# Optimization experiments

Measured on AMD Instinct MI355X. Metric: run time of the kernel, lower is better.

The kernel has to match this reference:

```python
import jax, jax.numpy as jnp
import numpy as np
import math

B, L, D = 2, 2048, 1024
H, HD = 16, 64          # num heads, head dim
R = 256                 # kv lora rank = D // 4
E, K, F = 8, 2, 1024    # routed experts, top_k, intermediate size


def rmsnorm(x, w, eps=1e-6):
    ms = jnp.mean(x * x, axis=-1, keepdims=True)
    return w * (x * jax.lax.rsqrt(ms + eps))


def setup_inputs() -> dict:
    key = jax.random.key(0)
    ks = jax.random.split(key, 16)
    s = 0.02
    return {
        "x": jax.random.normal(ks[0], (B, L, D), jnp.float32),
        "ln1_w": jnp.ones((D,), jnp.float32),
        "q_w": jax.random.normal(ks[1], (D, H * HD), jnp.float32) * s,
        "kvd_w": jax.random.normal(ks[2], (D, R), jnp.float32) * s,
        "kvn_w": jnp.ones((R,), jnp.float32),
        "kvu_w": jax.random.normal(ks[3], (R, 2 * H * HD), jnp.float32) * s,
        "o_w": jax.random.normal(ks[4], (H * HD, D), jnp.float32) * s,
        "ln2_w": jnp.ones((D,), jnp.float32),
        "gate_w": jax.random.normal(ks[5], (D, E), jnp.float32) * s,
        "sh_w1": jax.random.normal(ks[6], (D, F), jnp.float32) * s,
        "sh_w2": jax.random.normal(ks[7], (F, D), jnp.float32) * s,
        "sh_w3": jax.random.normal(ks[8], (D, F), jnp.float32) * s,
        "re_w1": jax.random.normal(ks[9], (E, D, F), jnp.float32) * s,
        "re_w2": jax.random.normal(ks[10], (E, F, D), jnp.float32) * s,
        "re_w3": jax.random.normal(ks[11], (E, D, F), jnp.float32) * s,
    }


def reference(x, ln1_w, q_w, kvd_w, kvn_w, kvu_w, o_w, ln2_w, gate_w,
              sh_w1, sh_w2, sh_w3, re_w1, re_w2, re_w3):
    # ---- MLHA attention with pre-RMSNorm and latent-compressed KV ----
    xn = rmsnorm(x, ln1_w)
    q = (xn @ q_w).reshape(B, L, H, HD)
    latent = rmsnorm(xn @ kvd_w, kvn_w)                 # [B,L,R]
    kv = latent @ kvu_w                                 # [B,L,2*H*HD]
    k, v = jnp.split(kv, 2, axis=-1)
    k = k.reshape(B, L, H, HD)
    v = v.reshape(B, L, H, HD)
    scores = jnp.einsum('bxhd,byhd->bhxy', q, k) / math.sqrt(HD)
    causal = jnp.tril(jnp.ones((L, L), bool))
    scores = jnp.where(causal, scores, -jnp.inf)
    attn = jax.nn.softmax(scores, axis=-1)
    attn_out = jnp.einsum('bhxy,byhd->bxhd', attn, v).reshape(B, L, H * HD)
    h = x + attn_out @ o_w

    # ---- MoE (inference: no jitter, expert_bias = 0, no bias update) ----
    hn = rmsnorm(h, ln2_w)
    flat = hn.reshape(-1, D)                            # [T,D], T=B*L
    # shared expert (SwiGLU)
    shared = (jax.nn.silu(flat @ sh_w1) * (flat @ sh_w3)) @ sh_w2
    # router
    logits = flat @ gate_w                              # [T,E]
    probs = jax.nn.softmax(logits, axis=-1)
    topw, topi = jax.lax.top_k(probs, K)                # [T,K]
    topw = topw / jnp.sum(topw, axis=-1, keepdims=True)
    # per-token per-expert combine weight [T,E]
    combine = jnp.sum(topw[..., None] * jax.nn.one_hot(topi, E, dtype=flat.dtype), axis=1)
    # all routed experts densely, then masked combine (same math as masked loop)
    h1 = jnp.einsum('td,edf->etf', flat, re_w1)
    h3 = jnp.einsum('td,edf->etf', flat, re_w3)
    eo = jnp.einsum('etf,efd->etd', jax.nn.silu(h1) * h3, re_w2)
    routed = jnp.einsum('te,etd->td', combine, eo)
    moe_out = (shared + routed).reshape(B, L, D)
    return h + moe_out, probs
```

## Files before the change

kernel.cpp:

```cpp
#include <hip/hip_runtime.h>
#include <hip/hip_bf16.h>
#include <cstdint>
#include <cstddef>

typedef unsigned short u16;
typedef unsigned int u32;
typedef __attribute__((ext_vector_type(8))) short bf16x8;
typedef __attribute__((ext_vector_type(4))) float f32x4;

static constexpr int Bb = 2, Ll = 2048, Dd = 1024, Hh = 16, Rr = 256, Ee = 8, Ff = 1024;
static constexpr int Tt = Bb * Ll;

__device__ __forceinline__ u16 f2bf(float f){
  union { float f; u32 u; } v; v.f = f;
  u32 u = v.u;
  u32 r = u + 0x7FFFu + ((u >> 16) & 1u);
  return (u16)(r >> 16);
}
__device__ __forceinline__ float bf2f(u16 b){
  union { u32 u; float f; } v; v.u = ((u32)b) << 16; return v.f;
}

#define GLDS(gp, lp) __builtin_amdgcn_global_load_lds( \
    (const __attribute__((address_space(1))) unsigned int*)(gp), \
    (__attribute__((address_space(3))) unsigned int*)(lp), 16, 0, 0)

__global__ void transpose_conv(const float* __restrict__ src, u16* __restrict__ dst,
                               int K, int N, int SN, int dstOff){
  __shared__ float tile[32][33];
  const float* s = src + (size_t)blockIdx.z * K * N;
  int bx = blockIdx.x * 32;
  int by = blockIdx.y * 32;
  int tx = threadIdx.x, ty = threadIdx.y;
  #pragma unroll
  for (int i = ty; i < 32; i += 8) tile[i][tx] = s[(size_t)(by + i) * N + bx + tx];
  __syncthreads();
  size_t rowbase = (size_t)blockIdx.z * SN + dstOff + bx;
  #pragma unroll
  for (int i = ty; i < 32; i += 8) dst[(rowbase + i) * K + by + tx] = f2bf(tile[tx][i]);
}

template<int DIM>
__global__ void rmsnorm_kernel(const float* __restrict__ x, const float* __restrict__ w,
                               u16* __restrict__ out){
  int t = blockIdx.x;
  const float* xr = x + (size_t)t * DIM;
  u16* orow = out + (size_t)t * DIM;
  int tid = threadIdx.x;
  constexpr int NT = 256;
  constexpr int PER = DIM / NT > 0 ? DIM / NT : 1;
  float vals[PER];
  float ss = 0.f;
  #pragma unroll
  for (int i = 0; i < PER; i++){
    int d = tid + i * NT;
    float v = (d < DIM) ? xr[d] : 0.f;
    vals[i] = v; ss += v * v;
  }
  __shared__ float red[4];
  for (int m = 32; m; m >>= 1) ss += __shfl_xor(ss, m, 64);
  if ((tid & 63) == 0) red[tid >> 6] = ss;
  __syncthreads();
  float tot = red[0] + red[1] + red[2] + red[3];
  float rn = rsqrtf(tot / DIM + 1e-6f);
  #pragma unroll
  for (int i = 0; i < PER; i++){
    int d = tid + i * NT;
    if (d < DIM) orow[d] = f2bf(vals[i] * rn * w[d]);
  }
}

__global__ void router_kernel(const float* __restrict__ h, const float* __restrict__ ln2w,
                              const float* __restrict__ gate,
                              float* __restrict__ probs_out,
                              int* __restrict__ topi, float* __restrict__ topw){
  int t = blockIdx.x; int tid = threadIdx.x;
  const float* hr = h + (size_t)t * Dd;
  float v[4]; float ss = 0.f;
  #pragma unroll
  for (int i = 0; i < 4; i++){ float x = hr[tid + i * 256]; v[i] = x; ss += x * x; }
  __shared__ float red[4];
  for (int m = 32; m; m >>= 1) ss += __shfl_xor(ss, m, 64);
  if ((tid & 63) == 0) red[tid >> 6] = ss;
  __syncthreads();
  float rn = rsqrtf((red[0] + red[1] + red[2] + red[3]) / Dd + 1e-6f);
  float p[8];
  #pragma unroll
  for (int e = 0; e < 8; e++) p[e] = 0.f;
  #pragma unroll
  for (int i = 0; i < 4; i++){
    int d = tid + i * 256;
    float hv = v[i] * rn * ln2w[d];
    const float* g = gate + (size_t)d * 8;
    #pragma unroll
    for (int e = 0; e < 8; e++) p[e] += hv * g[e];
  }
  #pragma unroll
  for (int e = 0; e < 8; e++){
    float x = p[e];
    for (int m = 32; m; m >>= 1) x += __shfl_xor(x, m, 64);
    p[e] = x;
  }
  __shared__ float pe[4][8];
  if ((tid & 63) == 0){ for (int e = 0; e < 8; e++) pe[tid >> 6][e] = p[e]; }
  __syncthreads();
  if (tid == 0){
    float lg[8];
    for (int e = 0; e < 8; e++) lg[e] = pe[0][e] + pe[1][e] + pe[2][e] + pe[3][e];
    float mx = lg[0];
    for (int e = 1; e < 8; e++) mx = fmaxf(mx, lg[e]);
    float pr[8]; float s = 0.f;
    for (int e = 0; e < 8; e++){ pr[e] = __expf(lg[e] - mx); s += pr[e]; }
    float inv = 1.f / s;
    for (int e = 0; e < 8; e++) probs_out[(size_t)t * 8 + e] = pr[e] * inv;
    int i0 = 0;
    for (int e = 1; e < 8; e++) if (pr[e] > pr[i0]) i0 = e;
    int i1 = -1;
    for (int e = 0; e < 8; e++){ if (e == i0) continue; if (i1 < 0 || pr[e] > pr[i1]) i1 = e; }
    float w0 = pr[i0], w1 = pr[i1]; float wn = 1.f / (w0 + w1);
    topi[t * 2] = i0; topi[t * 2 + 1] = i1;
    topw[t * 2] = w0 * wn; topw[t * 2 + 1] = w1 * wn;
  }
}

__global__ void hist_kernel(const int* __restrict__ topi, int* __restrict__ counts){
  __shared__ int h[8];
  int tid = threadIdx.x;
  if (tid < 8) h[tid] = 0;
  __syncthreads();
  int base = blockIdx.x * 512;
  for (int i = tid; i < 512; i += 256) atomicAdd(&h[topi[base + i]], 1);
  __syncthreads();
  if (tid < 8) atomicAdd(&counts[tid], h[tid]);
}

__global__ void scan_kernel(const int* __restrict__ counts, int* __restrict__ offs){
  if (threadIdx.x == 0 && blockIdx.x == 0){
    int c = 0;
    for (int e = 0; e < 8; e++){ offs[e] = c; c += counts[e]; }
  }
}

__global__ void bucket_kernel(const int* __restrict__ topi, const float* __restrict__ topw,
                              const int* __restrict__ offs, int* __restrict__ cur,
                              int* __restrict__ entries, float* __restrict__ ew){
  __shared__ int lh[8], lbase[8], lcur[8];
  int tid = threadIdx.x;
  if (tid < 8) lh[tid] = 0;
  __syncthreads();
  int t = blockIdx.x * 256 + tid;
  int e0 = topi[t * 2], e1 = topi[t * 2 + 1];
  atomicAdd(&lh[e0], 1); atomicAdd(&lh[e1], 1);
  __syncthreads();
  if (tid < 8){ lbase[tid] = atomicAdd(&cur[tid], lh[tid]); lcur[tid] = 0; }
  __syncthreads();
  int p0 = atomicAdd(&lcur[e0], 1);
  int pos0 = offs[e0] + lbase[e0] + p0;
  entries[pos0] = t; ew[pos0] = topw[t * 2];
  int p1 = atomicAdd(&lcur[e1], 1);
  int pos1 = offs[e1] + lbase[e1] + p1;
  entries[pos1] = t; ew[pos1] = topw[t * 2 + 1];
}

__global__ void swiglu_kernel(u16* __restrict__ buf, int rows){
  int idx = blockIdx.x * 256 + threadIdx.x;
  int t = idx >> 7, f = (idx & 127) * 8;
  if (t >= rows) return;
  u16* p = buf + (size_t)t * 2048 + f;
  bf16x8 a = *(const bf16x8*)p;
  bf16x8 b = *(const bf16x8*)(p + 1024);
  bf16x8 o;
  #pragma unroll
  for (int j = 0; j < 8; j++){
    float av = bf2f(((const u16*)&a)[j]);
    float bv = bf2f(((const u16*)&b)[j]);
    float s = av / (1.f + __expf(-av));
    ((u16*)&o)[j] = f2bf(s * bv);
  }
  *(bf16x8*)p = o;
}

template<int TM, int ROWMODE, int MODE>
__launch_bounds__(256)
__global__ void gemm_bt(const u16* __restrict__ A, const u16* __restrict__ Bt,
                        void* __restrict__ C, const float* __restrict__ res,
                        int M, int N, int K, int lda, int ldc,
                        const int* __restrict__ entries, const float* __restrict__ ew,
                        const int* __restrict__ counts, const int* __restrict__ offs,
                        float* __restrict__ outAt){
  constexpr int MTC = TM / 32;
  __shared__ __align__(16) u16 As[TM * 32];
  __shared__ __align__(16) u16 Bs[128 * 32];
  __shared__ int els[TM];
  __shared__ float ewl[TM];

  int e = (ROWMODE ? blockIdx.z : 0);
  const u16* Bte = Bt + (size_t)e * N * K;
  int cnt, off;
  if (ROWMODE == 0){ cnt = M; off = 0; }
  else { cnt = counts[e]; off = offs[e]; }
  int rt = blockIdx.y * TM;
  if (rt >= cnt) return;
  int cb = blockIdx.x * 128;
  int tid = threadIdx.x;

  if (ROWMODE >= 1){
    if (tid < TM){
      int r = rt + tid;
      els[tid] = (r < cnt) ? entries[off + r] : 0;
      ewl[tid] = (MODE == 4 && r < cnt) ? ew[off + r] : 0.f;
    }
    __syncthreads();
  }

  int sr = tid >> 2;
  int skc = (tid & 3) * 8;
  int rr0 = rt + sr, rr1 = rt + sr + 64;
  size_t ar0 = 0, ar1 = 0;
  if (ROWMODE == 0){ ar0 = (size_t)rr0; ar1 = (size_t)rr1; }
  else if (ROWMODE == 1){ ar0 = (size_t)els[sr];
                          ar1 = (TM == 128) ? (size_t)els[sr + 64] : 0; }
  else {
    int c0 = rr0 < cnt ? rr0 : (cnt - 1);
    int c1 = rr1 < cnt ? rr1 : (cnt - 1);
    ar0 = (size_t)off + c0; ar1 = (size_t)off + c1;
  }
  const u16* pa0 = A + ar0 * lda + skc;
  const u16* pa1 = A + ar1 * lda + skc;
  const u16* pb0 = Bte + (size_t)(cb + sr) * K + skc;
  const u16* pb1 = Bte + (size_t)(cb + sr + 64) * K + skc;
  u16* lA0 = &As[tid * 8];
  u16* lA1 = &As[(TM == 128 ? 2048 : 0) + tid * 8];
  u16* lB0 = &Bs[tid * 8];
  u16* lB1 = &Bs[2048 + tid * 8];

  int w = tid >> 6, lane = tid & 63;
  int wm = w >> 1, wn = w & 1;
  int quad = lane >> 4, l16 = lane & 15;

  f32x4 acc[MTC][4];
  const f32x4 zf = {0.f, 0.f, 0.f, 0.f};
  #pragma unroll
  for (int i = 0; i < MTC; i++)
    #pragma unroll
    for (int j = 0; j < 4; j++) acc[i][j] = zf;

  for (int k0 = 0; k0 < K; k0 += 32){
    __syncthreads();
    GLDS(pa0 + k0, lA0);
    if (TM == 128) GLDS(pa1 + k0, lA1);
    GLDS(pb0 + k0, lB0);
    GLDS(pb1 + k0, lB1);
    __syncthreads();
    bf16x8 af[MTC], bfr[4];
    #pragma unroll
    for (int mt = 0; mt < MTC; mt++)
      af[mt] = *(const bf16x8*)&As[(wm * (TM / 2) + mt * 16 + l16) * 32 + quad * 8];
    #pragma unroll
    for (int nt = 0; nt < 4; nt++)
      bfr[nt] = *(const bf16x8*)&Bs[(wn * 64 + nt * 16 + l16) * 32 + quad * 8];
    #pragma unroll
    for (int mt = 0; mt < MTC; mt++)
      #pragma unroll
      for (int nt = 0; nt < 4; nt++)
        acc[mt][nt] = __builtin_amdgcn_mfma_f32_16x16x32_bf16(af[mt], bfr[nt], acc[mt][nt], 0, 0, 0);
  }

  #pragma unroll
  for (int mt = 0; mt < MTC; mt++){
    #pragma unroll
    for (int nt = 0; nt < 4; nt++){
      #pragma unroll
      for (int r = 0; r < 4; r++){
        int row = wm * (TM / 2) + mt * 16 + quad * 4 + r;
        int col = cb + wn * 64 + nt * 16 + l16;
        int rr = rt + row;
        if (rr >= cnt) continue;
        float v = acc[mt][nt][r];
        if (MODE == 0){
          size_t ci = (size_t)((ROWMODE == 1) ? (off + rr) : rr) * ldc + col;
          ((u16*)C)[ci] = f2bf(v);
        } else if (MODE == 1){
          size_t ci = (size_t)rr * ldc + col;
          ((float*)C)[ci] = v + res[ci];
        } else if (MODE == 5){
          if (col < 1024) ((u16*)C)[(size_t)rr * 1024 + col] = f2bf(v);
          else            outAt[(size_t)rr * 256 + (col - 1024)] = v;
        } else {
          int tok = els[row];
          atomicAdd(&outAt[(size_t)tok * ldc + col], ewl[row] * v);
        }
      }
    }
  }
}

__global__ void vt_kernel(const u16* __restrict__ kv, u16* __restrict__ vt){
  __shared__ __align__(16) u16 t[64 * 72];
  int kt = blockIdx.x * 64, h = blockIdx.y, b = blockIdx.z;
  size_t bL = (size_t)b * Ll;
  int tid = threadIdx.x;
  int r = tid >> 2, c0 = (tid & 3) * 16;
  const u16* src = kv + (bL + kt + r) * 2048 + 1024 + h * 64 + c0;
  *(uint4*)&t[r * 72 + c0]     = *(const uint4*)(src);
  *(uint4*)&t[r * 72 + c0 + 8] = *(const uint4*)(src + 8);
  __syncthreads();
  int d = tid >> 2; int k0 = (tid & 3) * 16;
  u16 tmp[16];
  #pragma unroll
  for (int j = 0; j < 16; j++) tmp[j] = t[(k0 + j) * 72 + d];
  u16* dst = vt + ((size_t)(b * Hh + h) * 64 + d) * (size_t)Ll + kt + k0;
  *(uint4*)dst       = *(const uint4*)&tmp[0];
  *(uint4*)(dst + 8) = *(const uint4*)&tmp[8];
}

__launch_bounds__(256)
__global__ void attn_kernel(const u16* __restrict__ q, const u16* __restrict__ kv,
                            const u16* __restrict__ vt, u16* __restrict__ out){
  constexpr int LD = 72;
  __shared__ __align__(16) u16 Ks[64 * LD];
  __shared__ __align__(16) u16 Vs[64 * LD];
  __shared__ __align__(16) u16 Ps[64 * LD];
  int q0 = blockIdx.x * 64, h = blockIdx.y, b = blockIdx.z;
  size_t bL = (size_t)b * Ll;
  int tid = threadIdx.x, w = tid >> 6, lane = tid & 63, quad = lane >> 4, l16 = lane & 15;
  int qrow = q0 + w * 16 + l16;

  bf16x8 qf[2];
  #pragma unroll
  for (int ks = 0; ks < 2; ks++)
    qf[ks] = *(const bf16x8*)(q + (bL + qrow) * 1024 + h * 64 + ks * 32 + quad * 8);

  f32x4 oacc[4];
  const f32x4 zf = {0.f, 0.f, 0.f, 0.f};
  #pragma unroll
  for (int dt = 0; dt < 4; dt++) oacc[dt] = zf;
  float mprev = -1e30f, lsum = 0.f;

  int sr = tid >> 2, sc = (tid & 3) * 16;
  const u16* kbase = kv + (bL + sr) * 2048 + h * 64 + sc;
  const u16* vbase = vt + ((size_t)(b * Hh + h) * 64 + sr) * (size_t)Ll + sc;

  for (int kt = 0; kt <= q0; kt += 64){
    __syncthreads();
    {
      const u16* kp = kbase + (size_t)kt * 2048;
      *(uint4*)&Ks[sr * LD + sc]     = *(const uint4*)(kp);
      *(uint4*)&Ks[sr * LD + sc + 8] = *(const uint4*)(kp + 8);
      const u16* vp = vbase + kt;
      *(uint4*)&Vs[sr * LD + sc]     = *(const uint4*)(vp);
      *(uint4*)&Vs[sr * LD + sc + 8] = *(const uint4*)(vp + 8);
    }
    __syncthreads();

    f32x4 sacc[4];
    #pragma unroll
    for (int mt = 0; mt < 4; mt++) sacc[mt] = zf;
    #pragma unroll
    for (int ks = 0; ks < 2; ks++){
      #pragma unroll
      for (int mt = 0; mt < 4; mt++){
        bf16x8 kf = *(const bf16x8*)&Ks[(mt * 16 + l16) * LD + ks * 32 + quad * 8];
        sacc[mt] = __builtin_amdgcn_mfma_f32_16x16x32_bf16(kf, qf[ks], sacc[mt], 0, 0, 0);
      }
    }
    bool diag = (kt == q0);
    int lq = w * 16 + l16;
    float sv[16]; float mx = -1e30f;
    #pragma unroll
    for (int mt = 0; mt < 4; mt++){
      #pragma unroll
      for (int r = 0; r < 4; r++){
        float s = sacc[mt][r] * 0.125f;
        if (diag && (mt * 16 + quad * 4 + r > lq)) s = -1e30f;
        sv[mt * 4 + r] = s;
        mx = fmaxf(mx, s);
      }
    }
    mx = fmaxf(mx, __shfl_xor(mx, 16, 64));
    mx = fmaxf(mx, __shfl_xor(mx, 32, 64));
    float mnew = fmaxf(mprev, mx);
    float alpha = __expf(mprev - mnew);
    mprev = mnew;
    float rs = 0.f;
    #pragma unroll
    for (int mt = 0; mt < 4; mt++){
      ushort4 pk;
      float p0 = __expf(sv[mt * 4 + 0] - mnew);
      float p1 = __expf(sv[mt * 4 + 1] - mnew);
      float p2 = __expf(sv[mt * 4 + 2] - mnew);
      float p3 = __expf(sv[mt * 4 + 3] - mnew);
      rs += p0 + p1 + p2 + p3;
      pk.x = f2bf(p0); pk.y = f2bf(p1); pk.z = f2bf(p2); pk.w = f2bf(p3);
      *(ushort4*)&Ps[(w * 16 + l16) * LD + mt * 16 + quad * 4] = pk;
    }
    rs += __shfl_xor(rs, 16, 64);
    rs += __shfl_xor(rs, 32, 64);
    lsum = lsum * alpha + rs;
    #pragma unroll
    for (int dt = 0; dt < 4; dt++) oacc[dt] *= alpha;

    #pragma unroll
    for (int ks = 0; ks < 2; ks++){
      bf16x8 pf = *(const bf16x8*)&Ps[(w * 16 + l16) * LD + ks * 32 + quad * 8];
      #pragma unroll
      for (int dt = 0; dt < 4; dt++){
        bf16x8 vf = *(const bf16x8*)&Vs[(dt * 16 + l16) * LD + ks * 32 + quad * 8];
        oacc[dt] = __builtin_amdgcn_mfma_f32_16x16x32_bf16(vf, pf, oacc[dt], 0, 0, 0);
      }
    }
  }

  float inv = 1.f / lsum;
  #pragma unroll
  for (int dt = 0; dt < 4; dt++){
    ushort4 ov;
    ov.x = f2bf(oacc[dt][0] * inv);
    ov.y = f2bf(oacc[dt][1] * inv);
    ov.z = f2bf(oacc[dt][2] * inv);
    ov.w = f2bf(oacc[dt][3] * inv);
    *(ushort4*)(out + (bL + qrow) * 1024 + h * 64 + dt * 16 + quad * 4) = ov;
  }
}

extern "C" void kernel_launch(void* const* d_in, const int* in_sizes, int n_in,
                              void* d_out, int out_size, void* d_ws, size_t ws_size,
                              hipStream_t stream){
  const float* x     = (const float*)d_in[0];
  const float* ln1_w = (const float*)d_in[1];
  const float* q_w   = (const float*)d_in[2];
  const float* kvd_w = (const float*)d_in[3];
  const float* kvn_w = (const float*)d_in[4];
  const float* kvu_w = (const float*)d_in[5];
  const float* o_w   = (const float*)d_in[6];
  const float* ln2_w = (const float*)d_in[7];
  const float* gate_w= (const float*)d_in[8];
  const float* sh_w1 = (const float*)d_in[9];
  const float* sh_w2 = (const float*)d_in[10];
  const float* sh_w3 = (const float*)d_in[11];
  const float* re_w1 = (const float*)d_in[12];
  const float* re_w2 = (const float*)d_in[13];
  const float* re_w3 = (const float*)d_in[14];
  float* out = (float*)d_out;

  char* wp = (char*)d_ws;
  auto alloc = [&](size_t bytes)->char*{
    char* p = wp; wp += (bytes + 255) & ~(size_t)255; return p;
  };
  u16* qkvdT = (u16*)alloc((size_t)1280 * 1024 * 2);
  u16* kvuT  = (u16*)alloc((size_t)2048 * 256 * 2);
  u16* oT    = (u16*)alloc((size_t)1024 * 1024 * 2);
  u16* sh13T = (u16*)alloc((size_t)2048 * 1024 * 2);
  u16* sh2T  = (u16*)alloc((size_t)1024 * 1024 * 2);
  u16* re13T = (u16*)alloc((size_t)8 * 2048 * 1024 * 2);
  u16* re2T  = (u16*)alloc((size_t)8 * 1024 * 1024 * 2);
  u16* xn    = (u16*)alloc((size_t)Tt * 1024 * 2);
  u16* qbuf  = (u16*)alloc((size_t)Tt * 1024 * 2);
  float* latpre = (float*)alloc((size_t)Tt * 256 * 4);
  u16* lat   = (u16*)alloc((size_t)Tt * 256 * 2);
  u16* kvbuf = (u16*)alloc((size_t)Tt * 2048 * 2);
  u16* attnb = (u16*)alloc((size_t)Tt * 1024 * 2);
  float* hbuf = (float*)alloc((size_t)Tt * 1024 * 4);
  u16* vtb   = (u16*)alloc((size_t)Bb * Hh * 64 * Ll * 2);
  u16* h13r  = (u16*)alloc((size_t)Tt * 2 * 2048 * 2);
  int* counts = (int*)alloc(32);
  int* cur    = (int*)alloc(32);
  int* offs   = (int*)alloc(32);
  int* topi   = (int*)alloc((size_t)Tt * 2 * 4);
  float* topw = (float*)alloc((size_t)Tt * 2 * 4);
  int* entries= (int*)alloc((size_t)Tt * 2 * 4);
  float* ewt  = (float*)alloc((size_t)Tt * 2 * 4);
  (void)ws_size; (void)n_in; (void)in_sizes; (void)out_size;

  hipMemsetAsync(counts, 0, 32, stream);
  hipMemsetAsync(cur, 0, 32, stream);

  dim3 tb(32, 8);
  transpose_conv<<<dim3(32, 32, 1), tb, 0, stream>>>(q_w,   qkvdT, 1024, 1024, 1280, 0);
  transpose_conv<<<dim3(8,  32, 1), tb, 0, stream>>>(kvd_w, qkvdT, 1024, 256,  1280, 1024);
  transpose_conv<<<dim3(64, 8,  1), tb, 0, stream>>>(kvu_w, kvuT,  256,  2048, 2048, 0);
  transpose_conv<<<dim3(32, 32, 1), tb, 0, stream>>>(o_w,   oT,    1024, 1024, 1024, 0);
  transpose_conv<<<dim3(32, 32, 1), tb, 0, stream>>>(sh_w1, sh13T, 1024, 1024, 2048, 0);
  transpose_conv<<<dim3(32, 32, 1), tb, 0, stream>>>(sh_w3, sh13T, 1024, 1024, 2048, 1024);
  transpose_conv<<<dim3(32, 32, 1), tb, 0, stream>>>(sh_w2, sh2T,  1024, 1024, 1024, 0);
  transpose_conv<<<dim3(32, 32, 8), tb, 0, stream>>>(re_w1, re13T, 1024, 1024, 2048, 0);
  transpose_conv<<<dim3(32, 32, 8), tb, 0, stream>>>(re_w3, re13T, 1024, 1024, 2048, 1024);
  transpose_conv<<<dim3(32, 32, 8), tb, 0, stream>>>(re_w2, re2T,  1024, 1024, 1024, 0);

  rmsnorm_kernel<1024><<<Tt, 256, 0, stream>>>(x, ln1_w, xn);

  gemm_bt<64,0,5><<<dim3(10, 64), 256, 0, stream>>>(xn, qkvdT, qbuf, nullptr,
      Tt, 1280, 1024, 1024, 1024, nullptr, nullptr, nullptr, nullptr, latpre);
  rmsnorm_kernel<256><<<Tt, 256, 0, stream>>>(latpre, kvn_w, lat);
  gemm_bt<128,0,0><<<dim3(16, 32), 256, 0, stream>>>(lat, kvuT, kvbuf, nullptr,
      Tt, 2048, 256, 256, 2048, nullptr, nullptr, nullptr, nullptr, nullptr);
  vt_kernel<<<dim3(32, 16, 2), 256, 0, stream>>>(kvbuf, vtb);
  attn_kernel<<<dim3(32, 16, 2), 256, 0, stream>>>(qbuf, kvbuf, vtb, attnb);
  gemm_bt<64,0,1><<<dim3(8, 64), 256, 0, stream>>>(attnb, oT, hbuf, x,
      Tt, 1024, 1024, 1024, 1024, nullptr, nullptr, nullptr, nullptr, nullptr);
  rmsnorm_kernel<1024><<<Tt, 256, 0, stream>>>(hbuf, ln2_w, xn);
  router_kernel<<<Tt, 256, 0, stream>>>(hbuf, ln2_w, gate_w, out + (size_t)Tt * Dd,
                                        topi, topw);
  hist_kernel<<<16, 256, 0, stream>>>(topi, counts);
  scan_kernel<<<1, 64, 0, stream>>>(counts, offs);
  bucket_kernel<<<16, 256, 0, stream>>>(topi, topw, offs, cur, entries, ewt);

  gemm_bt<128,0,0><<<dim3(16, 32), 256, 0, stream>>>(xn, sh13T, kvbuf, nullptr,
      Tt, 2048, 1024, 1024, 2048, nullptr, nullptr, nullptr, nullptr, nullptr);
  swiglu_kernel<<<Tt / 2, 256, 0, stream>>>(kvbuf, Tt);
  gemm_bt<64,0,1><<<dim3(8, 64), 256, 0, stream>>>(kvbuf, sh2T, out, hbuf,
      Tt, 1024, 1024, 2048, 1024, nullptr, nullptr, nullptr, nullptr, nullptr);

  gemm_bt<128,1,0><<<dim3(16, 32, 8), 256, 0, stream>>>(xn, re13T, h13r, nullptr,
      Tt, 2048, 1024, 1024, 2048, entries, nullptr, counts, offs, nullptr);
  swiglu_kernel<<<Tt, 256, 0, stream>>>(h13r, 2 * Tt);
  gemm_bt<128,2,4><<<dim3(8, 32, 8), 256, 0, stream>>>(h13r, re2T, nullptr, nullptr,
      Tt, 1024, 1024, 2048, 1024, entries, ewt, counts, offs, out);
}
```

Before: 608.6 us.

## Fuse SwiGLU into GEMM epilogues, merge transposes, balance causal attention blocks

```diff
diff --git a/kernel.cpp b/kernel.cpp
--- a/kernel.cpp
+++ b/kernel.cpp
@@ -25,19 +25,61 @@
     (const __attribute__((address_space(1))) unsigned int*)(gp), \
     (__attribute__((address_space(3))) unsigned int*)(lp), 16, 0, 0)
 
+__global__ void transpose5(const float* __restrict__ q_w, const float* __restrict__ o_w,
+                           const float* __restrict__ w1, const float* __restrict__ w3,
+                           const float* __restrict__ w2,
+                           u16* __restrict__ qkvdT, u16* __restrict__ oT,
+                           u16* __restrict__ sh13T, u16* __restrict__ sh2T){
+  const float* s; u16* d; int off, str;
+  switch (blockIdx.z){
+    case 0: s = q_w; d = qkvdT; off = 0; str = 1; break;
+    case 1: s = o_w; d = oT;    off = 0; str = 1; break;
+    case 2: s = w1;  d = sh13T; off = 0; str = 2; break;
+    case 3: s = w3;  d = sh13T; off = 1; str = 2; break;
+    default: s = w2; d = sh2T;  off = 0; str = 1; break;
+  }
+  __shared__ float tile[32][33];
+  int bx = blockIdx.x * 32, by = blockIdx.y * 32;
+  int tx = threadIdx.x, ty = threadIdx.y;
+  #pragma unroll
+  for (int i = ty; i < 32; i += 8) tile[i][tx] = s[(size_t)(by + i) * 1024 + bx + tx];
+  __syncthreads();
+  #pragma unroll
+  for (int i = ty; i < 32; i += 8)
+    d[(size_t)(off + (bx + i) * str) * 1024 + by + tx] = f2bf(tile[tx][i]);
+}
+
+__global__ void transposeEx(const float* __restrict__ re_w1, const float* __restrict__ re_w3,
+                            const float* __restrict__ re_w2,
+                            u16* __restrict__ re13T, u16* __restrict__ re2T){
+  int z = blockIdx.z, which = z >> 3, e = z & 7;
+  const float* s; u16* d; int off, str;
+  size_t eo = (size_t)e * 1024 * 1024;
+  if (which == 0){ s = re_w1 + eo; d = re13T + (size_t)e * 2048 * 1024; off = 0; str = 2; }
+  else if (which == 1){ s = re_w3 + eo; d = re13T + (size_t)e * 2048 * 1024; off = 1; str = 2; }
+  else { s = re_w2 + eo; d = re2T + (size_t)e * 1024 * 1024; off = 0; str = 1; }
+  __shared__ float tile[32][33];
+  int bx = blockIdx.x * 32, by = blockIdx.y * 32;
+  int tx = threadIdx.x, ty = threadIdx.y;
+  #pragma unroll
+  for (int i = ty; i < 32; i += 8) tile[i][tx] = s[(size_t)(by + i) * 1024 + bx + tx];
+  __syncthreads();
+  #pragma unroll
+  for (int i = ty; i < 32; i += 8)
+    d[(size_t)(off + (bx + i) * str) * 1024 + by + tx] = f2bf(tile[tx][i]);
+}
+
 __global__ void transpose_conv(const float* __restrict__ src, u16* __restrict__ dst,
-                               int K, int N, int SN, int dstOff){
+                               int K, int N, int dstOff){
   __shared__ float tile[32][33];
-  const float* s = src + (size_t)blockIdx.z * K * N;
-  int bx = blockIdx.x * 32;
-  int by = blockIdx.y * 32;
+  int bx = blockIdx.x * 32, by = blockIdx.y * 32;
   int tx = threadIdx.x, ty = threadIdx.y;
   #pragma unroll
-  for (int i = ty; i < 32; i += 8) tile[i][tx] = s[(size_t)(by + i) * N + bx + tx];
-  __syncthreads();
-  size_t rowbase = (size_t)blockIdx.z * SN + dstOff + bx;
-  #pragma unroll
-  for (int i = ty; i < 32; i += 8) dst[(rowbase + i) * K + by + tx] = f2bf(tile[tx][i]);
+  for (int i = ty; i < 32; i += 8) tile[i][tx] = src[(size_t)(by + i) * N + bx + tx];
+  __syncthreads();
+  #pragma unroll
+  for (int i = ty; i < 32; i += 8)
+    dst[(size_t)(dstOff + bx + i) * K + by + tx] = f2bf(tile[tx][i]);
 }
 
 template<int DIM>
@@ -73,7 +115,8 @@
 __global__ void router_kernel(const float* __restrict__ h, const float* __restrict__ ln2w,
                               const float* __restrict__ gate,
                               float* __restrict__ probs_out,
-                              int* __restrict__ topi, float* __restrict__ topw){
+                              int* __restrict__ topi, float* __restrict__ topw,
+                              u16* __restrict__ hn){
   int t = blockIdx.x; int tid = threadIdx.x;
   const float* hr = h + (size_t)t * Dd;
   float v[4]; float ss = 0.f;
@@ -91,6 +134,7 @@
   for (int i = 0; i < 4; i++){
     int d = tid + i * 256;
     float hv = v[i] * rn * ln2w[d];
+    hn[(size_t)t * Dd + d] = f2bf(hv);
     const float* g = gate + (size_t)d * 8;
     #pragma unroll
     for (int e = 0; e < 8; e++) p[e] += hv * g[e];
@@ -134,17 +178,10 @@
   if (tid < 8) atomicAdd(&counts[tid], h[tid]);
 }
 
-__global__ void scan_kernel(const int* __restrict__ counts, int* __restrict__ offs){
-  if (threadIdx.x == 0 && blockIdx.x == 0){
-    int c = 0;
-    for (int e = 0; e < 8; e++){ offs[e] = c; c += counts[e]; }
-  }
-}
-
 __global__ void bucket_kernel(const int* __restrict__ topi, const float* __restrict__ topw,
-                              const int* __restrict__ offs, int* __restrict__ cur,
+                              const int* __restrict__ counts, int* __restrict__ cur,
                               int* __restrict__ entries, float* __restrict__ ew){
-  __shared__ int lh[8], lbase[8], lcur[8];
+  __shared__ int lh[8], lbase[8], lcur[8], loffs[8];
   int tid = threadIdx.x;
   if (tid < 8) lh[tid] = 0;
   __syncthreads();
@@ -152,32 +189,18 @@
   int e0 = topi[t * 2], e1 = topi[t * 2 + 1];
   atomicAdd(&lh[e0], 1); atomicAdd(&lh[e1], 1);
   __syncthreads();
+  if (tid == 0){
+    int c = 0;
+    for (int e = 0; e < 8; e++){ loffs[e] = c; c += counts[e]; }
+  }
   if (tid < 8){ lbase[tid] = atomicAdd(&cur[tid], lh[tid]); lcur[tid] = 0; }
   __syncthreads();
   int p0 = atomicAdd(&lcur[e0], 1);
-  int pos0 = offs[e0] + lbase[e0] + p0;
+  int pos0 = loffs[e0] + lbase[e0] + p0;
   entries[pos0] = t; ew[pos0] = topw[t * 2];
   int p1 = atomicAdd(&lcur[e1], 1);
-  int pos1 = offs[e1] + lbase[e1] + p1;
+  int pos1 = loffs[e1] + lbase[e1] + p1;
   entries[pos1] = t; ew[pos1] = topw[t * 2 + 1];
-}
-
-__global__ void swiglu_kernel(u16* __restrict__ buf, int rows){
-  int idx = blockIdx.x * 256 + threadIdx.x;
-  int t = idx >> 7, f = (idx & 127) * 8;
-  if (t >= rows) return;
-  u16* p = buf + (size_t)t * 2048 + f;
-  bf16x8 a = *(const bf16x8*)p;
-  bf16x8 b = *(const bf16x8*)(p + 1024);
-  bf16x8 o;
-  #pragma unroll
-  for (int j = 0; j < 8; j++){
-    float av = bf2f(((const u16*)&a)[j]);
-    float bv = bf2f(((const u16*)&b)[j]);
-    float s = av / (1.f + __expf(-av));
-    ((u16*)&o)[j] = f2bf(s * bv);
-  }
-  *(bf16x8*)p = o;
 }
 
 template<int TM, int ROWMODE, int MODE>
@@ -186,7 +209,7 @@
                         void* __restrict__ C, const float* __restrict__ res,
                         int M, int N, int K, int lda, int ldc,
                         const int* __restrict__ entries, const float* __restrict__ ew,
-                        const int* __restrict__ counts, const int* __restrict__ offs,
+                        const int* __restrict__ counts,
                         float* __restrict__ outAt){
   constexpr int MTC = TM / 32;
   __shared__ __align__(16) u16 As[TM * 32];
@@ -198,7 +221,11 @@
   const u16* Bte = Bt + (size_t)e * N * K;
   int cnt, off;
   if (ROWMODE == 0){ cnt = M; off = 0; }
-  else { cnt = counts[e]; off = offs[e]; }
+  else {
+    cnt = counts[e];
+    off = 0;
+    for (int i = 0; i < e; i++) off += counts[i];
+  }
   int rt = blockIdx.y * TM;
   if (rt >= cnt) return;
   int cb = blockIdx.x * 128;
@@ -275,8 +302,17 @@
         int row = wm * (TM / 2) + mt * 16 + quad * 4 + r;
         int col = cb + wn * 64 + nt * 16 + l16;
         int rr = rt + row;
+        float v = acc[mt][nt][r];
+        if (MODE == 6){
+          float pv = __shfl_xor(v, 1, 64);
+          if (rr < cnt && (l16 & 1) == 0){
+            float sl = v / (1.f + __expf(-v));
+            size_t crow = (size_t)((ROWMODE == 1) ? (off + rr) : rr);
+            ((u16*)C)[crow * ldc + (col >> 1)] = f2bf(sl * pv);
+          }
+          continue;
+        }
         if (rr >= cnt) continue;
-        float v = acc[mt][nt][r];
         if (MODE == 0){
           size_t ci = (size_t)((ROWMODE == 1) ? (off + rr) : rr) * ldc + col;
           ((u16*)C)[ci] = f2bf(v);
@@ -318,108 +354,112 @@
 __global__ void attn_kernel(const u16* __restrict__ q, const u16* __restrict__ kv,
                             const u16* __restrict__ vt, u16* __restrict__ out){
   constexpr int LD = 72;
+  const float CS = 0.18033688011112042f;
   __shared__ __align__(16) u16 Ks[64 * LD];
   __shared__ __align__(16) u16 Vs[64 * LD];
   __shared__ __align__(16) u16 Ps[64 * LD];
-  int q0 = blockIdx.x * 64, h = blockIdx.y, b = blockIdx.z;
+  int h = blockIdx.y, b = blockIdx.z;
   size_t bL = (size_t)b * Ll;
   int tid = threadIdx.x, w = tid >> 6, lane = tid & 63, quad = lane >> 4, l16 = lane & 15;
-  int qrow = q0 + w * 16 + l16;
-
-  bf16x8 qf[2];
-  #pragma unroll
-  for (int ks = 0; ks < 2; ks++)
-    qf[ks] = *(const bf16x8*)(q + (bL + qrow) * 1024 + h * 64 + ks * 32 + quad * 8);
-
-  f32x4 oacc[4];
-  const f32x4 zf = {0.f, 0.f, 0.f, 0.f};
-  #pragma unroll
-  for (int dt = 0; dt < 4; dt++) oacc[dt] = zf;
-  float mprev = -1e30f, lsum = 0.f;
-
   int sr = tid >> 2, sc = (tid & 3) * 16;
   const u16* kbase = kv + (bL + sr) * 2048 + h * 64 + sc;
   const u16* vbase = vt + ((size_t)(b * Hh + h) * 64 + sr) * (size_t)Ll + sc;
-
-  for (int kt = 0; kt <= q0; kt += 64){
-    __syncthreads();
-    {
-      const u16* kp = kbase + (size_t)kt * 2048;
-      *(uint4*)&Ks[sr * LD + sc]     = *(const uint4*)(kp);
-      *(uint4*)&Ks[sr * LD + sc + 8] = *(const uint4*)(kp + 8);
-      const u16* vp = vbase + kt;
-      *(uint4*)&Vs[sr * LD + sc]     = *(const uint4*)(vp);
-      *(uint4*)&Vs[sr * LD + sc + 8] = *(const uint4*)(vp + 8);
-    }
-    __syncthreads();
-
-    f32x4 sacc[4];
-    #pragma unroll
-    for (int mt = 0; mt < 4; mt++) sacc[mt] = zf;
-    #pragma unroll
-    for (int ks = 0; ks < 2; ks++){
+  const f32x4 zf = {0.f, 0.f, 0.f, 0.f};
+
+  #pragma unroll
+  for (int pass = 0; pass < 2; pass++){
+    int q0 = (pass ? (31 - (int)blockIdx.x) : (int)blockIdx.x) * 64;
+    int qrow = q0 + w * 16 + l16;
+
+    bf16x8 qf[2];
+    #pragma unroll
+    for (int ks = 0; ks < 2; ks++)
+      qf[ks] = *(const bf16x8*)(q + (bL + qrow) * 1024 + h * 64 + ks * 32 + quad * 8);
+
+    f32x4 oacc[4];
+    #pragma unroll
+    for (int dt = 0; dt < 4; dt++) oacc[dt] = zf;
+    float mprev = -1e30f, lsum = 0.f;
+
+    for (int kt = 0; kt <= q0; kt += 64){
+      __syncthreads();
+      {
+        const u16* kp = kbase + (size_t)kt * 2048;
+        *(uint4*)&Ks[sr * LD + sc]     = *(const uint4*)(kp);
+        *(uint4*)&Ks[sr * LD + sc + 8] = *(const uint4*)(kp + 8);
+        const u16* vp = vbase + kt;
+        *(uint4*)&Vs[sr * LD + sc]     = *(const uint4*)(vp);
+        *(uint4*)&Vs[sr * LD + sc + 8] = *(const uint4*)(vp + 8);
+      }
+      __syncthreads();
+
+      f32x4 sacc[4];
+      #pragma unroll
+      for (int mt = 0; mt < 4; mt++) sacc[mt] = zf;
+      #pragma unroll
+      for (int ks = 0; ks < 2; ks++){
+        #pragma unroll
+        for (int mt = 0; mt < 4; mt++){
+          bf16x8 kf = *(const bf16x8*)&Ks[(mt * 16 + l16) * LD + ks * 32 + quad * 8];
+          sacc[mt] = __builtin_amdgcn_mfma_f32_16x16x32_bf16(kf, qf[ks], sacc[mt], 0, 0, 0);
+        }
+      }
+      bool diag = (kt == q0);
+      int lq = w * 16 + l16;
+      float sv[16]; float mx = -1e30f;
       #pragma unroll
       for (int mt = 0; mt < 4; mt++){
-        bf16x8 kf = *(const bf16x8*)&Ks[(mt * 16 + l16) * LD + ks * 32 + quad * 8];
-        sacc[mt] = __builtin_amdgcn_mfma_f32_16x16x32_bf16(kf, qf[ks], sacc[mt], 0, 0, 0);
+        #pragma unroll
+        for (int r = 0; r < 4; r++){
+          float s = sacc[mt][r] * CS;
+          if (diag && (mt * 16 + quad * 4 + r > lq)) s = -1e30f;
+          sv[mt * 4 + r] = s;
+          mx = fmaxf(mx, s);
+        }
+      }
+      mx = fmaxf(mx, __shfl_xor(mx, 16, 64));
+      mx = fmaxf(mx, __shfl_xor(mx, 32, 64));
+      float mnew = fmaxf(mprev, mx);
+      float alpha = exp2f(mprev - mnew);
+      mprev = mnew;
+      float rs = 0.f;
+      #pragma unroll
+      for (int mt = 0; mt < 4; mt++){
+        float p0 = exp2f(sv[mt * 4 + 0] - mnew);
+        float p1 = exp2f(sv[mt * 4 + 1] - mnew);
+        float p2 = exp2f(sv[mt * 4 + 2] - mnew);
+        float p3 = exp2f(sv[mt * 4 + 3] - mnew);
+        rs += p0 + p1 + p2 + p3;
+        union { uint2 u; __hip_bfloat162 h2[2]; } pk;
+        pk.h2[0] = __float22bfloat162_rn(make_float2(p0, p1));
+        pk.h2[1] = __float22bfloat162_rn(make_float2(p2, p3));
+        *(uint2*)&Ps[(w * 16 + l16) * LD + mt * 16 + quad * 4] = pk.u;
+      }
+      rs += __shfl_xor(rs, 16, 64);
+      rs += __shfl_xor(rs, 32, 64);
+      lsum = lsum * alpha + rs;
+      #pragma unroll
+      for (int dt = 0; dt < 4; dt++) oacc[dt] *= alpha;
+
+      #pragma unroll
+      for (int ks = 0; ks < 2; ks++){
+        bf16x8 pf = *(const bf16x8*)&Ps[(w * 16 + l16) * LD + ks * 32 + quad * 8];
+        #pragma unroll
+        for (int dt = 0; dt < 4; dt++){
+          bf16x8 vf = *(const bf16x8*)&Vs[(dt * 16 + l16) * LD + ks * 32 + quad * 8];
+          oacc[dt] = __builtin_amdgcn_mfma_f32_16x16x32_bf16(vf, pf, oacc[dt], 0, 0, 0);
+        }
       }
     }
-    bool diag = (kt == q0);
-    int lq = w * 16 + l16;
-    float sv[16]; float mx = -1e30f;
-    #pragma unroll
-    for (int mt = 0; mt < 4; mt++){
-      #pragma unroll
-      for (int r = 0; r < 4; r++){
-        float s = sacc[mt][r] * 0.125f;
-        if (diag && (mt * 16 + quad * 4 + r > lq)) s = -1e30f;
-        sv[mt * 4 + r] = s;
-        mx = fmaxf(mx, s);
-      }
+
+    float inv = 1.f / lsum;
+    #pragma unroll
+    for (int dt = 0; dt < 4; dt++){
+      union { uint2 u; __hip_bfloat162 h2[2]; } ov;
+      ov.h2[0] = __float22bfloat162_rn(make_float2(oacc[dt][0] * inv, oacc[dt][1] * inv));
+      ov.h2[1] = __float22bfloat162_rn(make_float2(oacc[dt][2] * inv, oacc[dt][3] * inv));
+      *(uint2*)(out + (bL + qrow) * 1024 + h * 64 + dt * 16 + quad * 4) = ov.u;
     }
-    mx = fmaxf(mx, __shfl_xor(mx, 16, 64));
-    mx = fmaxf(mx, __shfl_xor(mx, 32, 64));
-    float mnew = fmaxf(mprev, mx);
-    float alpha = __expf(mprev - mnew);
-    mprev = mnew;
-    float rs = 0.f;
-    #pragma unroll
-    for (int mt = 0; mt < 4; mt++){
-      ushort4 pk;
-      float p0 = __expf(sv[mt * 4 + 0] - mnew);
-      float p1 = __expf(sv[mt * 4 + 1] - mnew);
-      float p2 = __expf(sv[mt * 4 + 2] - mnew);
-      float p3 = __expf(sv[mt * 4 + 3] - mnew);
-      rs += p0 + p1 + p2 + p3;
-      pk.x = f2bf(p0); pk.y = f2bf(p1); pk.z = f2bf(p2); pk.w = f2bf(p3);
-      *(ushort4*)&Ps[(w * 16 + l16) * LD + mt * 16 + quad * 4] = pk;
-    }
-    rs += __shfl_xor(rs, 16, 64);
-    rs += __shfl_xor(rs, 32, 64);
-    lsum = lsum * alpha + rs;
-    #pragma unroll
-    for (int dt = 0; dt < 4; dt++) oacc[dt] *= alpha;
-
-    #pragma unroll
-    for (int ks = 0; ks < 2; ks++){
-      bf16x8 pf = *(const bf16x8*)&Ps[(w * 16 + l16) * LD + ks * 32 + quad * 8];
-      #pragma unroll
-      for (int dt = 0; dt < 4; dt++){
-        bf16x8 vf = *(const bf16x8*)&Vs[(dt * 16 + l16) * LD + ks * 32 + quad * 8];
-        oacc[dt] = __builtin_amdgcn_mfma_f32_16x16x32_bf16(vf, pf, oacc[dt], 0, 0, 0);
-      }
-    }
-  }
-
-  float inv = 1.f / lsum;
-  #pragma unroll
-  for (int dt = 0; dt < 4; dt++){
-    ushort4 ov;
-    ov.x = f2bf(oacc[dt][0] * inv);
-    ov.y = f2bf(oacc[dt][1] * inv);
-    ov.z = f2bf(oacc[dt][2] * inv);
-    ov.w = f2bf(oacc[dt][3] * inv);
-    *(ushort4*)(out + (bL + qrow) * 1024 + h * 64 + dt * 16 + quad * 4) = ov;
   }
 }
 
@@ -462,10 +502,9 @@
   u16* attnb = (u16*)alloc((size_t)Tt * 1024 * 2);
   float* hbuf = (float*)alloc((size_t)Tt * 1024 * 4);
   u16* vtb   = (u16*)alloc((size_t)Bb * Hh * 64 * Ll * 2);
-  u16* h13r  = (u16*)alloc((size_t)Tt * 2 * 2048 * 2);
+  u16* gr    = (u16*)alloc((size_t)Tt * 2 * 1024 * 2);
   int* counts = (int*)alloc(32);
   int* cur    = (int*)alloc(32);
-  int* offs   = (int*)alloc(32);
   int* topi   = (int*)alloc((size_t)Tt * 2 * 4);
   float* topw = (float*)alloc((size_t)Tt * 2 * 4);
   int* entries= (int*)alloc((size_t)Tt * 2 * 4);
@@ -476,44 +515,35 @@
   hipMemsetAsync(cur, 0, 32, stream);
 
   dim3 tb(32, 8);
-  transpose_conv<<<dim3(32, 32, 1), tb, 0, stream>>>(q_w,   qkvdT, 1024, 1024, 1280, 0);
-  transpose_conv<<<dim3(8,  32, 1), tb, 0, stream>>>(kvd_w, qkvdT, 1024, 256,  1280, 1024);
-  transpose_conv<<<dim3(64, 8,  1), tb, 0, stream>>>(kvu_w, kvuT,  256,  2048, 2048, 0);
-  transpose_conv<<<dim3(32, 32, 1), tb, 0, stream>>>(o_w,   oT,    1024, 1024, 1024, 0);
-  transpose_conv<<<dim3(32, 32, 1), tb, 0, stream>>>(sh_w1, sh13T, 1024, 1024, 2048, 0);
-  transpose_conv<<<dim3(32, 32, 1), tb, 0, stream>>>(sh_w3, sh13T, 1024, 1024, 2048, 1024);
-  transpose_conv<<<dim3(32, 32, 1), tb, 0, stream>>>(sh_w2, sh2T,  1024, 1024, 1024, 0);
-  transpose_conv<<<dim3(32, 32, 8), tb, 0, stream>>>(re_w1, re13T, 1024, 1024, 2048, 0);
-  transpose_conv<<<dim3(32, 32, 8), tb, 0, stream>>>(re_w3, re13T, 1024, 1024, 2048, 1024);
-  transpose_conv<<<dim3(32, 32, 8), tb, 0, stream>>>(re_w2, re2T,  1024, 1024, 1024, 0);
+  transpose5<<<dim3(32, 32, 5), tb, 0, stream>>>(q_w, o_w, sh_w1, sh_w3, sh_w2,
+                                                 qkvdT, oT, sh13T, sh2T);
+  transpose_conv<<<dim3(8, 32, 1), tb, 0, stream>>>(kvd_w, qkvdT, 1024, 256, 1024);
+  transpose_conv<<<dim3(64, 8, 1), tb, 0, stream>>>(kvu_w, kvuT, 256, 2048, 0);
+  transposeEx<<<dim3(32, 32, 24), tb, 0, stream>>>(re_w1, re_w3, re_w2, re13T, re2T);
 
   rmsnorm_kernel<1024><<<Tt, 256, 0, stream>>>(x, ln1_w, xn);
 
   gemm_bt<64,0,5><<<dim3(10, 64), 256, 0, stream>>>(xn, qkvdT, qbuf, nullptr,
-      Tt, 1280, 1024, 1024, 1024, nullptr, nullptr, nullptr, nullptr, latpre);
+      Tt, 1280, 1024, 1024, 1024, nullptr, nullptr, nullptr, latpre);
   rmsnorm_kernel<256><<<Tt, 256, 0, stream>>>(latpre, kvn_w, lat);
   gemm_bt<128,0,0><<<dim3(16, 32), 256, 0, stream>>>(lat, kvuT, kvbuf, nullptr,
-      Tt, 2048, 256, 256, 2048, nullptr, nullptr, nullptr, nullptr, nullptr);
+      Tt, 2048, 256, 256, 2048, nullptr, nullptr, nullptr, nullptr);
   vt_kernel<<<dim3(32, 16, 2), 256, 0, stream>>>(kvbuf, vtb);
-  attn_kernel<<<dim3(32, 16, 2), 256, 0, stream>>>(qbuf, kvbuf, vtb, attnb);
+  attn_kernel<<<dim3(16, 16, 2), 256, 0, stream>>>(qbuf, kvbuf, vtb, attnb);
   gemm_bt<64,0,1><<<dim3(8, 64), 256, 0, stream>>>(attnb, oT, hbuf, x,
-      Tt, 1024, 1024, 1024, 1024, nullptr, nullptr, nullptr, nullptr, nullptr);
-  rmsnorm_kernel<1024><<<Tt, 256, 0, stream>>>(hbuf, ln2_w, xn);
+      Tt, 1024, 1024, 1024, 1024, nullptr, nullptr, nullptr, nullptr);
   router_kernel<<<Tt, 256, 0, stream>>>(hbuf, ln2_w, gate_w, out + (size_t)Tt * Dd,
-                                        topi, topw);
+                                        topi, topw, xn);
   hist_kernel<<<16, 256, 0, stream>>>(topi, counts);
-  scan_kernel<<<1, 64, 0, stream>>>(counts, offs);
-  bucket_kernel<<<16, 256, 0, stream>>>(topi, topw, offs, cur, entries, ewt);
-
-  gemm_bt<128,0,0><<<dim3(16, 32), 256, 0, stream>>>(xn, sh13T, kvbuf, nullptr,
-      Tt, 2048, 1024, 1024, 2048, nullptr, nullptr, nullptr, nullptr, nullptr);
-  swiglu_kernel<<<Tt / 2, 256, 0, stream>>>(kvbuf, Tt);
+  bucket_kernel<<<16, 256, 0, stream>>>(topi, topw, counts, cur, entries, ewt);
+
+  gemm_bt<128,0,6><<<dim3(16, 32), 256, 0, stream>>>(xn, sh13T, kvbuf, nullptr,
+      Tt, 2048, 1024, 1024, 1024, nullptr, nullptr, nullptr, nullptr);
   gemm_bt<64,0,1><<<dim3(8, 64), 256, 0, stream>>>(kvbuf, sh2T, out, hbuf,
-      Tt, 1024, 1024, 2048, 1024, nullptr, nullptr, nullptr, nullptr, nullptr);
-
-  gemm_bt<128,1,0><<<dim3(16, 32, 8), 256, 0, stream>>>(xn, re13T, h13r, nullptr,
-      Tt, 2048, 1024, 1024, 2048, entries, nullptr, counts, offs, nullptr);
-  swiglu_kernel<<<Tt, 256, 0, stream>>>(h13r, 2 * Tt);
-  gemm_bt<128,2,4><<<dim3(8, 32, 8), 256, 0, stream>>>(h13r, re2T, nullptr, nullptr,
-      Tt, 1024, 1024, 2048, 1024, entries, ewt, counts, offs, out);
-}
+      Tt, 1024, 1024, 1024, 1024, nullptr, nullptr, nullptr, nullptr);
+
+  gemm_bt<128,1,6><<<dim3(16, 32, 8), 256, 0, stream>>>(xn, re13T, gr, nullptr,
+      Tt, 2048, 1024, 1024, 1024, entries, nullptr, counts, nullptr);
+  gemm_bt<128,2,4><<<dim3(8, 32, 8), 256, 0, stream>>>(gr, re2T, nullptr, nullptr,
+      Tt, 1024, 1024, 1024, 1024, entries, ewt, counts, out);
+}
```

Result: faster. 580.3 us (-4.6%).
